# Kernel optimization log

Hardware: AMD Instinct MI355X
Metric: run time of the kernel (lower is better)

## Reference

```python
import jax, jax.numpy as jnp
import numpy as np

NUM_HEADS = 16
HEAD_DIM = 64
Q_DIM = K_DIM = V_DIM = 1024
LQ = LK = 4096
TAU = HEAD_DIM ** (-0.5)


def setup_inputs() -> dict:
    key = jax.random.key(0)
    ks = jax.random.split(key, 11)
    inner = NUM_HEADS * HEAD_DIM
    s = 0.02
    return {
        "q": jax.random.normal(ks[0], (LQ, Q_DIM), dtype=jnp.float32),
        "k": jax.random.normal(ks[1], (LK, K_DIM), dtype=jnp.float32),
        "v": jax.random.normal(ks[2], (LK, V_DIM), dtype=jnp.float32),
        "Wq": jax.random.normal(ks[3], (Q_DIM, inner), dtype=jnp.float32) * s,
        "bq": jax.random.normal(ks[4], (inner,), dtype=jnp.float32) * s,
        "Wk": jax.random.normal(ks[5], (K_DIM, inner), dtype=jnp.float32) * s,
        "bk": jax.random.normal(ks[6], (inner,), dtype=jnp.float32) * s,
        "Wv": jax.random.normal(ks[7], (V_DIM, inner), dtype=jnp.float32) * s,
        "bv": jax.random.normal(ks[8], (inner,), dtype=jnp.float32) * s,
        "Wo": jax.random.normal(ks[9], (inner, Q_DIM), dtype=jnp.float32) * s,
        "bo": jax.random.normal(ks[10], (Q_DIM,), dtype=jnp.float32) * s,
    }


def reference(q, k, v, Wq, bq, Wk, bk, Wv, bv, Wo, bo):
    h, x = NUM_HEADS, HEAD_DIM
    # projections: [L, h*x] -> per-head layout
    qh = (q @ Wq + bq).reshape(-1, h, x)  # [Lq, h, x]
    kh = (k @ Wk + bk).reshape(-1, h, x)  # [Lk, h, x]
    vh = (v @ Wv + bv).reshape(-1, h, x)  # [Lk, h, x]
    # scores: [h, Lq, Lk]
    att = jnp.einsum('qhx,khx->hqk', qh, kh) * TAU
    att = jax.nn.softmax(att, axis=-1)  # dropout=0.0 -> identity
    ctx = jnp.einsum('hqk,khx->qhx', att, vh).reshape(-1, h * x)  # [Lq, h*x]
    out = ctx @ Wo + bo  # [Lq, Q_DIM]
    return out, att
```

## Files before the change

### kernel.cpp

```cpp
#include <hip/hip_runtime.h>
#include <hip/hip_bf16.h>

typedef unsigned short ushort_t;
typedef __attribute__((ext_vector_type(8))) short short8;
typedef __attribute__((ext_vector_type(8))) __bf16 bf16x8;
typedef __attribute__((ext_vector_type(4))) float f32x4;

#define LQS 4096
#define LKS 4096
#define NH 16
#define HD 64
#define DIN 1024
#define KVB 64
static constexpr float TAU_S = 0.125f;
static constexpr float LOG2E = 1.4426950408889634f;

__device__ __forceinline__ float exp2_fast(float x) { return __builtin_amdgcn_exp2f(x); }
__device__ __forceinline__ float log2_fast(float x) { return __builtin_amdgcn_logf(x); }

__device__ __forceinline__ ushort_t f32_to_bf16(float x) {
  union { float f; unsigned u; } v; v.f = x;
  unsigned r = v.u + 0x7FFF + ((v.u >> 16) & 1);
  return (ushort_t)(r >> 16);
}

__device__ __forceinline__ unsigned cvt_pk_bf16(float a, float b) {
  unsigned r;
  asm volatile("v_cvt_pk_bf16_f32 %0, %1, %2" : "=v"(r) : "v"(a), "v"(b));
  return r;
}

__device__ __forceinline__ void gld_lds16(const void* g, void* l) {
  __builtin_amdgcn_global_load_lds((const __attribute__((address_space(1))) void*)g,
                                   (__attribute__((address_space(3))) void*)l, 16, 0, 0);
}

__device__ __forceinline__ f32x4 mfma16(bf16x8 a, bf16x8 b, f32x4 c) {
  return __builtin_amdgcn_mfma_f32_16x16x32_bf16(a, b, c, 0, 0, 0);
}

struct Cvt3 { const float* src[3]; ushort_t* dst[3]; };
__global__ void cvt_kernel(Cvt3 c) {
  const float* __restrict__ src = c.src[blockIdx.y];
  ushort_t* __restrict__ dst = c.dst[blockIdx.y];
  int i = (blockIdx.x * 256 + threadIdx.x) * 8;
  float4 a = *(const float4*)(src + i);
  float4 b = *(const float4*)(src + i + 4);
  union { unsigned w[4]; short8 s; } o;
  o.w[0] = cvt_pk_bf16(a.x, a.y);
  o.w[1] = cvt_pk_bf16(a.z, a.w);
  o.w[2] = cvt_pk_bf16(b.x, b.y);
  o.w[3] = cvt_pk_bf16(b.z, b.w);
  *(short8*)(dst + i) = o.s;
}

struct TW4 { const float* W[4]; ushort_t* Wt[4]; };
__global__ void transpose_w(TW4 w) {
  const float* __restrict__ W = w.W[blockIdx.z];
  ushort_t* __restrict__ Wt = w.Wt[blockIdx.z];
  __shared__ float tile[64][65];
  const int t = threadIdx.x;
  const int k0 = blockIdx.y * 64, n0 = blockIdx.x * 64;
#pragma unroll
  for (int i = 0; i < 16; ++i) {
    int idx = i * 256 + t;
    int r = idx >> 6, c = idx & 63;
    tile[r][c] = W[(size_t)(k0 + r) * DIN + n0 + c];
  }
  __syncthreads();
#pragma unroll
  for (int i = 0; i < 16; ++i) {
    int idx = i * 256 + t;
    int r = idx >> 6, c = idx & 63;
    Wt[(size_t)(n0 + r) * DIN + k0 + c] = f32_to_bf16(tile[c][r]);
  }
}

__global__ void transpose_v(const ushort_t* __restrict__ vh, ushort_t* __restrict__ vt) {
  __shared__ ushort_t tile[64][65];
  const int t = threadIdx.x;
  const int k0 = blockIdx.x * 64, h = blockIdx.y;
#pragma unroll
  for (int i = 0; i < 16; ++i) {
    int idx = i * 256 + t;
    int r = idx >> 6, c = idx & 63;
    tile[r][c] = vh[(size_t)(k0 + r) * DIN + h * HD + c];
  }
  __syncthreads();
#pragma unroll
  for (int i = 0; i < 16; ++i) {
    int idx = i * 256 + t;
    int r = idx >> 6, c = idx & 63;
    vt[((size_t)h * HD + r) * (size_t)LKS + k0 + c] = tile[c][r];
  }
}

struct Batch3 {
  const ushort_t* A[3];
  const ushort_t* Bt[3];
  const float* bias[3];
  void* C[3];
  float scale[3];
};
template <bool OUT_F32>
__launch_bounds__(256, 2)
__global__ void gemm_nt(Batch3 bt3) {
  const int bid = blockIdx.x;
  const int xcd = bid & 7, idx = bid >> 3;
  const int z = idx >> 5, rem = idx & 31;
  const int by = xcd * 4 + (rem >> 3), bx = rem & 7;
  const ushort_t* __restrict__ A = bt3.A[z];
  const ushort_t* __restrict__ Bt = bt3.Bt[z];
  const float* __restrict__ bias = bt3.bias[z];
  void* __restrict__ Cout = bt3.C[z];
  const float scale = bt3.scale[z];
  const int K = DIN, N = DIN;

  __shared__ __align__(16) ushort_t Alds[128 * 64];
  __shared__ __align__(16) ushort_t Blds[128 * 64];
  const int t = threadIdx.x, wave = t >> 6, lane = t & 63;
  const int l15 = lane & 15, lg = lane >> 4;
  const int m0 = by * 128, n0 = bx * 128;
  const int wr = wave >> 1, wc = wave & 1;
  f32x4 acc[4][4];
#pragma unroll
  for (int i = 0; i < 4; ++i)
#pragma unroll
    for (int j = 0; j < 4; ++j) acc[i][j] = (f32x4){0.f, 0.f, 0.f, 0.f};

  for (int tk = 0; tk < K / 64; ++tk) {
#pragma unroll
    for (int c = 0; c < 4; ++c) {
      int chunk = wave * 4 + c;
      int row = chunk * 8 + (lane >> 3);
      int ss = (lane & 7) ^ (row & 7);
      gld_lds16(A + (size_t)(m0 + row) * K + tk * 64 + ss * 8, (char*)Alds + chunk * 1024);
      gld_lds16(Bt + (size_t)(n0 + row) * K + tk * 64 + ss * 8, (char*)Blds + chunk * 1024);
    }
    __syncthreads();
#pragma unroll
    for (int kk = 0; kk < 2; ++kk) {
      bf16x8 a[4], b[4];
#pragma unroll
      for (int i = 0; i < 4; ++i) {
        int ra = wr * 64 + i * 16 + l15;
        a[i] = *(const bf16x8*)((const char*)Alds + ra * 128 + ((((kk * 4 + lg) << 4)) ^ ((ra & 7) << 4)));
        int rb = wc * 64 + i * 16 + l15;
        b[i] = *(const bf16x8*)((const char*)Blds + rb * 128 + ((((kk * 4 + lg) << 4)) ^ ((rb & 7) << 4)));
      }
#pragma unroll
      for (int mi = 0; mi < 4; ++mi)
#pragma unroll
        for (int ni = 0; ni < 4; ++ni)
          acc[mi][ni] = mfma16(a[mi], b[ni], acc[mi][ni]);
    }
    __syncthreads();
  }
#pragma unroll
  for (int ni = 0; ni < 4; ++ni) {
    int coln = n0 + wc * 64 + ni * 16 + l15;
    float bv = bias[coln];
#pragma unroll
    for (int mi = 0; mi < 4; ++mi) {
#pragma unroll
      for (int r = 0; r < 4; ++r) {
        int rowm = m0 + wr * 64 + mi * 16 + lg * 4 + r;
        float v = (acc[mi][ni][r] + bv) * scale;
        if (OUT_F32)
          ((float*)Cout)[(size_t)rowm * N + coln] = v;
        else
          ((ushort_t*)Cout)[(size_t)rowm * N + coln] = f32_to_bf16(v);
      }
    }
  }
}

__launch_bounds__(256, 2)
__global__ void rowsum_kernel(const ushort_t* __restrict__ qh, const ushort_t* __restrict__ kh,
                              float* __restrict__ rsbuf) {
  __shared__ __align__(16) ushort_t Klds[2][KVB * 64];
  const int t = threadIdx.x, wave = t >> 6, lane = t & 63;
  const int l15 = lane & 15, lg = lane >> 4;
  const int bid = blockIdx.x;
  const int xcd = bid & 7, idx = bid >> 3;
  const int h = xcd * 2 + (idx >> 5);
  const int rem = idx & 31;
  const int q0 = (rem >> 1) * 256;
  const int half = rem & 1;
  const int w0 = q0 + wave * 64;

  bf16x8 qa[4][2];
#pragma unroll
  for (int g = 0; g < 4; ++g) {
    const ushort_t* qp = qh + (size_t)(w0 + g * 16 + l15) * DIN + h * HD + lg * 8;
    qa[g][0] = *(const bf16x8*)(qp);
    qa[g][1] = *(const bf16x8*)(qp + 32);
  }

  const int srow8 = lane >> 3;
  const int sslot = (lane & 7);
  const int tk0 = half * 32;

#define STAGE_K1(tile, buf)                                                         \
  {                                                                                 \
    _Pragma("unroll") for (int c = 0; c < 2; ++c) {                                 \
      int chunk = wave * 2 + c;                                                     \
      int row = chunk * 8 + srow8;                                                  \
      int ss = sslot ^ (row & 7);                                                   \
      gld_lds16(kh + (size_t)((tile) * KVB + row) * DIN + h * HD + ss * 8,          \
                (char*)Klds[buf] + chunk * 1024);                                   \
    }                                                                               \
  }

  float rs[4] = {0.f, 0.f, 0.f, 0.f};
  STAGE_K1(tk0, 0);
  __syncthreads();
  int cur = 0;
  for (int tk = 0; tk < 32; ++tk) {
    if (tk + 1 < 32) STAGE_K1(tk0 + tk + 1, cur ^ 1);
#pragma unroll
    for (int ct = 0; ct < 4; ++ct) {
      int row = ct * 16 + l15;
      bf16x8 kb0 = *(const bf16x8*)((const char*)Klds[cur] + row * 128 + (((lg << 4)) ^ ((row & 7) << 4)));
      bf16x8 kb1 = *(const bf16x8*)((const char*)Klds[cur] + row * 128 + ((((4 + lg) << 4)) ^ ((row & 7) << 4)));
      f32x4 a[4];
#pragma unroll
      for (int g = 0; g < 4; ++g) {
        a[g] = mfma16(kb0, qa[g][0], (f32x4){0.f, 0.f, 0.f, 0.f});
        a[g] = mfma16(kb1, qa[g][1], a[g]);
      }
#pragma unroll
      for (int g = 0; g < 4; ++g)
#pragma unroll
        for (int r = 0; r < 4; ++r) rs[g] += exp2_fast(a[g][r]);
    }
    __syncthreads();
    cur ^= 1;
  }
#undef STAGE_K1
#pragma unroll
  for (int g = 0; g < 4; ++g) {
    rs[g] += __shfl_xor(rs[g], 16, 64);
    rs[g] += __shfl_xor(rs[g], 32, 64);
  }
  if (lg == 0) {
#pragma unroll
    for (int g = 0; g < 4; ++g)
      rsbuf[(((size_t)half * NH + h) << 12) + w0 + g * 16 + l15] = rs[g];
  }
}

__launch_bounds__(256, 2)
__global__ void attn_kernel(const ushort_t* __restrict__ qh, const ushort_t* __restrict__ kh,
                            const ushort_t* __restrict__ vt, const float* __restrict__ rsbuf,
                            float* __restrict__ att, ushort_t* __restrict__ ctx) {
  __shared__ __align__(16) ushort_t Klds[2][KVB * 64];
  __shared__ __align__(16) ushort_t Vlds[2][KVB * 64];
  const int t = threadIdx.x, wave = t >> 6, lane = t & 63;
  const int l15 = lane & 15, lg = lane >> 4;
  const int bid = blockIdx.x;
  const int xcd = bid & 7, idx = bid >> 3;
  const int h = xcd * 2 + (idx >> 5);
  const int q0 = (idx & 31) * 128;
  const int w0 = q0 + wave * 32;

  bf16x8 qa[2][2];
#pragma unroll
  for (int g = 0; g < 2; ++g) {
    const ushort_t* qp = qh + (size_t)(w0 + g * 16 + l15) * DIN + h * HD + lg * 8;
    qa[g][0] = *(const bf16x8*)(qp);
    qa[g][1] = *(const bf16x8*)(qp + 32);
  }

  float lrs[2];
#pragma unroll
  for (int g = 0; g < 2; ++g) {
    size_t row = (size_t)w0 + g * 16 + l15;
    float ps = rsbuf[((size_t)h << 12) + row] + rsbuf[(((size_t)NH + h) << 12) + row];
    lrs[g] = log2_fast(ps);
  }

  const int srow8 = lane >> 3;
  const int sslot = (lane & 7);

  f32x4 cacc[2][4];
#pragma unroll
  for (int g = 0; g < 2; ++g)
#pragma unroll
    for (int x = 0; x < 4; ++x) cacc[g][x] = (f32x4){0.f, 0.f, 0.f, 0.f};
  float* atth = att + ((size_t)h << 24);

  for (int tk = 0; tk < LKS / (2 * KVB); ++tk) {
#pragma unroll
    for (int sub = 0; sub < 2; ++sub) {
#pragma unroll
      for (int c = 0; c < 2; ++c) {
        int chunk = wave * 2 + c;
        int row = chunk * 8 + srow8;
        int ss = sslot ^ (row & 7);
        gld_lds16(kh + (size_t)((tk * 2 + sub) * KVB + row) * DIN + h * HD + ss * 8,
                  (char*)Klds[sub] + chunk * 1024);
        gld_lds16(vt + ((size_t)h * HD + row) * (size_t)LKS + (tk * 2 + sub) * KVB + ss * 8,
                  (char*)Vlds[sub] + chunk * 1024);
      }
    }
    __syncthreads();
#pragma unroll
    for (int sub = 0; sub < 2; ++sub) {
      float p[2][4][4];
#pragma unroll
      for (int ct = 0; ct < 4; ++ct) {
        f32x4 a0 = (f32x4){0.f, 0.f, 0.f, 0.f};
        f32x4 a1 = (f32x4){0.f, 0.f, 0.f, 0.f};
#pragma unroll
        for (int kk = 0; kk < 2; ++kk) {
          int row = ct * 16 + l15;
          bf16x8 kb = *(const bf16x8*)((const char*)Klds[sub] + row * 128 + ((((kk * 4 + lg) << 4)) ^ ((row & 7) << 4)));
          a0 = mfma16(kb, qa[0][kk], a0);
          a1 = mfma16(kb, qa[1][kk], a1);
        }
#pragma unroll
        for (int r = 0; r < 4; ++r) {
          p[0][ct][r] = exp2_fast(a0[r] - lrs[0]);
          p[1][ct][r] = exp2_fast(a1[r] - lrs[1]);
        }
      }
#pragma unroll
      for (int g = 0; g < 2; ++g) {
#pragma unroll
        for (int ct = 0; ct < 4; ++ct) {
          f32x4 v = (f32x4){p[g][ct][0], p[g][ct][1], p[g][ct][2], p[g][ct][3]};
          *(f32x4*)(atth + (((size_t)(w0 + g * 16 + l15)) << 12) + (tk * 2 + sub) * KVB + ct * 16 + lg * 4) = v;
        }
      }
      bf16x8 pa[2][2];
#pragma unroll
      for (int g = 0; g < 2; ++g)
#pragma unroll
        for (int kk = 0; kk < 2; ++kk) {
          union { unsigned w[4]; bf16x8 v; } P;
          P.w[0] = cvt_pk_bf16(p[g][2 * kk][0], p[g][2 * kk][1]);
          P.w[1] = cvt_pk_bf16(p[g][2 * kk][2], p[g][2 * kk][3]);
          P.w[2] = cvt_pk_bf16(p[g][2 * kk + 1][0], p[g][2 * kk + 1][1]);
          P.w[3] = cvt_pk_bf16(p[g][2 * kk + 1][2], p[g][2 * kk + 1][3]);
          pa[g][kk] = P.v;
        }
#pragma unroll
      for (int x = 0; x < 4; ++x) {
        int row = x * 16 + l15;
        const char* vrow = (const char*)Vlds[sub] + row * 128;
        int par = row & 7;
        int sb = (lg & 1) << 3;
#pragma unroll
        for (int kk = 0; kk < 2; ++kk) {
          int sA = (4 * kk + (lg >> 1)) ^ par;
          int sB = (4 * kk + 2 + (lg >> 1)) ^ par;
          union { unsigned long long q[2]; bf16x8 v; } U;
          U.q[0] = *(const unsigned long long*)(vrow + (sA << 4) + sb);
          U.q[1] = *(const unsigned long long*)(vrow + (sB << 4) + sb);
          cacc[0][x] = mfma16(pa[0][kk], U.v, cacc[0][x]);
          cacc[1][x] = mfma16(pa[1][kk], U.v, cacc[1][x]);
        }
      }
    }
    __syncthreads();
  }
#pragma unroll
  for (int g = 0; g < 2; ++g)
#pragma unroll
    for (int x = 0; x < 4; ++x) {
#pragma unroll
      for (int r = 0; r < 4; ++r) {
        int rowq = w0 + g * 16 + lg * 4 + r;
        int col = h * HD + x * 16 + l15;
        ctx[(size_t)rowq * DIN + col] = f32_to_bf16(cacc[g][x][r]);
      }
    }
}

extern "C" void kernel_launch(void* const* d_in, const int* in_sizes, int n_in,
                              void* d_out, int out_size, void* d_ws, size_t ws_size,
                              hipStream_t stream) {
  const float* q = (const float*)d_in[0];
  const float* k = (const float*)d_in[1];
  const float* v = (const float*)d_in[2];
  const float* Wq = (const float*)d_in[3];
  const float* bq = (const float*)d_in[4];
  const float* Wk = (const float*)d_in[5];
  const float* bk = (const float*)d_in[6];
  const float* Wv = (const float*)d_in[7];
  const float* bv = (const float*)d_in[8];
  const float* Wo = (const float*)d_in[9];
  const float* bo = (const float*)d_in[10];

  float* out = (float*)d_out;
  float* att = out + (size_t)LQS * DIN;

  char* ws = (char*)d_ws;
  ushort_t* qhb = (ushort_t*)(ws + (size_t)0);
  ushort_t* khb = (ushort_t*)(ws + ((size_t)8 << 20));
  ushort_t* vhb = (ushort_t*)(ws + ((size_t)16 << 20));
  ushort_t* vtb = (ushort_t*)(ws + ((size_t)24 << 20));
  ushort_t* ctx = (ushort_t*)(ws + ((size_t)32 << 20));
  ushort_t* qb = (ushort_t*)(ws + ((size_t)40 << 20));
  ushort_t* kb = (ushort_t*)(ws + ((size_t)48 << 20));
  ushort_t* vb = (ushort_t*)(ws + ((size_t)56 << 20));
  ushort_t* Wqt = (ushort_t*)(ws + ((size_t)64 << 20));
  ushort_t* Wkt = (ushort_t*)(ws + ((size_t)66 << 20));
  ushort_t* Wvt = (ushort_t*)(ws + ((size_t)68 << 20));
  ushort_t* Wot = (ushort_t*)(ws + ((size_t)70 << 20));
  float* rsbuf = (float*)(ws + ((size_t)72 << 20));

  Cvt3 c3;
  c3.src[0] = q; c3.src[1] = k; c3.src[2] = v;
  c3.dst[0] = qb; c3.dst[1] = kb; c3.dst[2] = vb;
  cvt_kernel<<<dim3(LQS * DIN / 8 / 256, 3), 256, 0, stream>>>(c3);

  TW4 w4;
  w4.W[0] = Wq; w4.W[1] = Wk; w4.W[2] = Wv; w4.W[3] = Wo;
  w4.Wt[0] = Wqt; w4.Wt[1] = Wkt; w4.Wt[2] = Wvt; w4.Wt[3] = Wot;
  transpose_w<<<dim3(16, 16, 4), 256, 0, stream>>>(w4);

  Batch3 pb;
  pb.A[0] = qb; pb.A[1] = kb; pb.A[2] = vb;
  pb.Bt[0] = Wqt; pb.Bt[1] = Wkt; pb.Bt[2] = Wvt;
  pb.bias[0] = bq; pb.bias[1] = bk; pb.bias[2] = bv;
  pb.C[0] = qhb; pb.C[1] = khb; pb.C[2] = vhb;
  pb.scale[0] = TAU_S * LOG2E; pb.scale[1] = 1.0f; pb.scale[2] = 1.0f;
  gemm_nt<false><<<768, 256, 0, stream>>>(pb);

  rowsum_kernel<<<512, 256, 0, stream>>>(qhb, khb, rsbuf);

  transpose_v<<<dim3(64, 16), 256, 0, stream>>>(vhb, vtb);

  attn_kernel<<<512, 256, 0, stream>>>(qhb, khb, vtb, rsbuf, att, ctx);

  Batch3 ob;
  ob.A[0] = ctx; ob.A[1] = ctx; ob.A[2] = ctx;
  ob.Bt[0] = Wot; ob.Bt[1] = Wot; ob.Bt[2] = Wot;
  ob.bias[0] = bo; ob.bias[1] = bo; ob.bias[2] = bo;
  ob.C[0] = out; ob.C[1] = out; ob.C[2] = out;
  ob.scale[0] = 1.0f; ob.scale[1] = 1.0f; ob.scale[2] = 1.0f;
  gemm_nt<true><<<256, 256, 0, stream>>>(ob);
}
```

Baseline: 385.9 us.

## Split attention over key halves with fp32 partial context and combine kernel

The attention kernel now launches 1024 blocks, each handling half of the key range for a 128-row query tile. Because softmax normalisation comes from the precomputed row sums, the two partial context sums can simply be added. Partial contexts are written as fp32 to the workspace, and a new combine kernel sums them and converts to bf16. Launch bounds rise to 4 blocks per SM, and the probability-to-bf16 packing is interleaved per column tile to cut live registers. This aims for more parallelism and better latency hiding, at the cost of an extra 32MB fp32 write and read plus one more kernel launch.

```diff
diff --git a/kernel.cpp b/kernel.cpp
--- a/kernel.cpp
+++ b/kernel.cpp
@@ -52,6 +52,21 @@
   o.w[2] = cvt_pk_bf16(b.x, b.y);
   o.w[3] = cvt_pk_bf16(b.z, b.w);
   *(short8*)(dst + i) = o.s;
+}
+
+__global__ void combine_ctx(const float* __restrict__ p0, const float* __restrict__ p1,
+                            ushort_t* __restrict__ ctx) {
+  int i = (blockIdx.x * 256 + threadIdx.x) * 8;
+  float4 a0 = *(const float4*)(p0 + i);
+  float4 b0 = *(const float4*)(p0 + i + 4);
+  float4 a1 = *(const float4*)(p1 + i);
+  float4 b1 = *(const float4*)(p1 + i + 4);
+  union { unsigned w[4]; short8 s; } o;
+  o.w[0] = cvt_pk_bf16(a0.x + a1.x, a0.y + a1.y);
+  o.w[1] = cvt_pk_bf16(a0.z + a1.z, a0.w + a1.w);
+  o.w[2] = cvt_pk_bf16(b0.x + b1.x, b0.y + b1.y);
+  o.w[3] = cvt_pk_bf16(b0.z + b1.z, b0.w + b1.w);
+  *(short8*)(ctx + i) = o.s;
 }
 
 struct TW4 { const float* W[4]; ushort_t* Wt[4]; };
@@ -250,18 +265,20 @@
   }
 }
 
-__launch_bounds__(256, 2)
+__launch_bounds__(256, 4)
 __global__ void attn_kernel(const ushort_t* __restrict__ qh, const ushort_t* __restrict__ kh,
                             const ushort_t* __restrict__ vt, const float* __restrict__ rsbuf,
-                            float* __restrict__ att, ushort_t* __restrict__ ctx) {
+                            float* __restrict__ att, float* __restrict__ pctx) {
   __shared__ __align__(16) ushort_t Klds[2][KVB * 64];
   __shared__ __align__(16) ushort_t Vlds[2][KVB * 64];
   const int t = threadIdx.x, wave = t >> 6, lane = t & 63;
   const int l15 = lane & 15, lg = lane >> 4;
   const int bid = blockIdx.x;
   const int xcd = bid & 7, idx = bid >> 3;
-  const int h = xcd * 2 + (idx >> 5);
-  const int q0 = (idx & 31) * 128;
+  const int h = xcd * 2 + (idx >> 6);
+  const int rem = idx & 63;
+  const int q0 = (rem >> 1) * 128;
+  const int half = rem & 1;
   const int w0 = q0 + wave * 32;
 
   bf16x8 qa[2][2];
@@ -282,6 +299,7 @@
 
   const int srow8 = lane >> 3;
   const int sslot = (lane & 7);
+  const int tb0 = half * 32;
 
   f32x4 cacc[2][4];
 #pragma unroll
@@ -290,7 +308,7 @@
     for (int x = 0; x < 4; ++x) cacc[g][x] = (f32x4){0.f, 0.f, 0.f, 0.f};
   float* atth = att + ((size_t)h << 24);
 
-  for (int tk = 0; tk < LKS / (2 * KVB); ++tk) {
+  for (int tk = 0; tk < 16; ++tk) {
 #pragma unroll
     for (int sub = 0; sub < 2; ++sub) {
 #pragma unroll
@@ -298,16 +316,17 @@
         int chunk = wave * 2 + c;
         int row = chunk * 8 + srow8;
         int ss = sslot ^ (row & 7);
-        gld_lds16(kh + (size_t)((tk * 2 + sub) * KVB + row) * DIN + h * HD + ss * 8,
+        gld_lds16(kh + (size_t)((tb0 + tk * 2 + sub) * KVB + row) * DIN + h * HD + ss * 8,
                   (char*)Klds[sub] + chunk * 1024);
-        gld_lds16(vt + ((size_t)h * HD + row) * (size_t)LKS + (tk * 2 + sub) * KVB + ss * 8,
+        gld_lds16(vt + ((size_t)h * HD + row) * (size_t)LKS + (tb0 + tk * 2 + sub) * KVB + ss * 8,
                   (char*)Vlds[sub] + chunk * 1024);
       }
     }
     __syncthreads();
 #pragma unroll
     for (int sub = 0; sub < 2; ++sub) {
-      float p[2][4][4];
+      bf16x8 pa[2][2];
+      float pprev[2][4];
 #pragma unroll
       for (int ct = 0; ct < 4; ++ct) {
         f32x4 a0 = (f32x4){0.f, 0.f, 0.f, 0.f};
@@ -319,32 +338,34 @@
           a0 = mfma16(kb, qa[0][kk], a0);
           a1 = mfma16(kb, qa[1][kk], a1);
         }
+        float pcur[2][4];
 #pragma unroll
         for (int r = 0; r < 4; ++r) {
-          p[0][ct][r] = exp2_fast(a0[r] - lrs[0]);
-          p[1][ct][r] = exp2_fast(a1[r] - lrs[1]);
+          pcur[0][r] = exp2_fast(a0[r] - lrs[0]);
+          pcur[1][r] = exp2_fast(a1[r] - lrs[1]);
         }
-      }
-#pragma unroll
-      for (int g = 0; g < 2; ++g) {
-#pragma unroll
-        for (int ct = 0; ct < 4; ++ct) {
-          f32x4 v = (f32x4){p[g][ct][0], p[g][ct][1], p[g][ct][2], p[g][ct][3]};
-          *(f32x4*)(atth + (((size_t)(w0 + g * 16 + l15)) << 12) + (tk * 2 + sub) * KVB + ct * 16 + lg * 4) = v;
+#pragma unroll
+        for (int g = 0; g < 2; ++g) {
+          f32x4 v = (f32x4){pcur[g][0], pcur[g][1], pcur[g][2], pcur[g][3]};
+          *(f32x4*)(atth + (((size_t)(w0 + g * 16 + l15)) << 12) + (tb0 + tk * 2 + sub) * KVB + ct * 16 + lg * 4) = v;
         }
-      }
-      bf16x8 pa[2][2];
-#pragma unroll
-      for (int g = 0; g < 2; ++g)
-#pragma unroll
-        for (int kk = 0; kk < 2; ++kk) {
-          union { unsigned w[4]; bf16x8 v; } P;
-          P.w[0] = cvt_pk_bf16(p[g][2 * kk][0], p[g][2 * kk][1]);
-          P.w[1] = cvt_pk_bf16(p[g][2 * kk][2], p[g][2 * kk][3]);
-          P.w[2] = cvt_pk_bf16(p[g][2 * kk + 1][0], p[g][2 * kk + 1][1]);
-          P.w[3] = cvt_pk_bf16(p[g][2 * kk + 1][2], p[g][2 * kk + 1][3]);
-          pa[g][kk] = P.v;
+        if (ct & 1) {
+#pragma unroll
+          for (int g = 0; g < 2; ++g) {
+            union { unsigned w[4]; bf16x8 v; } P;
+            P.w[0] = cvt_pk_bf16(pprev[g][0], pprev[g][1]);
+            P.w[1] = cvt_pk_bf16(pprev[g][2], pprev[g][3]);
+            P.w[2] = cvt_pk_bf16(pcur[g][0], pcur[g][1]);
+            P.w[3] = cvt_pk_bf16(pcur[g][2], pcur[g][3]);
+            pa[g][ct >> 1] = P.v;
+          }
+        } else {
+#pragma unroll
+          for (int g = 0; g < 2; ++g)
+#pragma unroll
+            for (int r = 0; r < 4; ++r) pprev[g][r] = pcur[g][r];
         }
+      }
 #pragma unroll
       for (int x = 0; x < 4; ++x) {
         int row = x * 16 + l15;
@@ -365,6 +386,7 @@
     }
     __syncthreads();
   }
+  float* pc = pctx + (size_t)half * LQS * DIN;
 #pragma unroll
   for (int g = 0; g < 2; ++g)
 #pragma unroll
@@ -373,7 +395,7 @@
       for (int r = 0; r < 4; ++r) {
         int rowq = w0 + g * 16 + lg * 4 + r;
         int col = h * HD + x * 16 + l15;
-        ctx[(size_t)rowq * DIN + col] = f32_to_bf16(cacc[g][x][r]);
+        pc[(size_t)rowq * DIN + col] = cacc[g][x][r];
       }
     }
 }
@@ -408,8 +430,9 @@
   ushort_t* Wqt = (ushort_t*)(ws + ((size_t)64 << 20));
   ushort_t* Wkt = (ushort_t*)(ws + ((size_t)66 << 20));
   ushort_t* Wvt = (ushort_t*)(ws + ((size_t)68 << 20));
-  ushort_t* Wot = (ushort_t*)(ws + ((size_t)70 << 20));
-  float* rsbuf = (float*)(ws + ((size_t)72 << 20));
+  float* pctx = (float*)(ws + ((size_t)40 << 20));
+  ushort_t* Wot = (ushort_t*)(ws + ((size_t)72 << 20));
+  float* rsbuf = (float*)(ws + ((size_t)74 << 20));
 
   Cvt3 c3;
   c3.src[0] = q; c3.src[1] = k; c3.src[2] = v;
@@ -433,7 +456,9 @@
 
   transpose_v<<<dim3(64, 16), 256, 0, stream>>>(vhb, vtb);
 
-  attn_kernel<<<512, 256, 0, stream>>>(qhb, khb, vtb, rsbuf, att, ctx);
+  attn_kernel<<<1024, 256, 0, stream>>>(qhb, khb, vtb, rsbuf, att, pctx);
+
+  combine_ctx<<<LQS * DIN / 8 / 256, 256, 0, stream>>>(pctx, pctx + (size_t)LQS * DIN, ctx);
 
   Batch3 ob;
   ob.A[0] = ctx; ob.A[1] = ctx; ob.A[2] = ctx;
```

Result: no change. 388.2 us (+0.6%).
